# Performance work log

Hardware: AMD Instinct MI355X
Metric: run time of the kernel (lower is better)

Reference implementation:

```python
import jax, jax.numpy as jnp
import numpy as np

KEY_CHANNELS = 256


def conv1x1_relu(x, w, b):
    # x: [B, Cin, H, W], w: [Cout, Cin], b: [Cout] -> [B, Cout, H, W]
    y = jnp.einsum('oc,bchw->bohw', w, x) + b[None, :, None, None]
    return jax.nn.relu(y)


def setup_inputs() -> dict:
    key = jax.random.key(0)
    ks = jax.random.split(key, 16)
    B, C, H, W = 8, 512, 128, 128
    Kc, Kp = KEY_CHANNELS, 150
    sc = lambda cin: 1.0 / np.sqrt(cin)
    return {
        'x': jax.random.normal(ks[0], (B, C, H, W), jnp.float32),
        'proxy': jax.random.normal(ks[1], (B, C, Kp, 1), jnp.float32),
        'w_fp1': jax.random.normal(ks[2], (Kc, C), jnp.float32) * sc(C),
        'b_fp1': jax.random.normal(ks[3], (Kc,), jnp.float32) * 0.1,
        'w_fp2': jax.random.normal(ks[4], (Kc, Kc), jnp.float32) * sc(Kc),
        'b_fp2': jax.random.normal(ks[5], (Kc,), jnp.float32) * 0.1,
        'w_fo1': jax.random.normal(ks[6], (Kc, C), jnp.float32) * sc(C),
        'b_fo1': jax.random.normal(ks[7], (Kc,), jnp.float32) * 0.1,
        'w_fo2': jax.random.normal(ks[8], (Kc, Kc), jnp.float32) * sc(Kc),
        'b_fo2': jax.random.normal(ks[9], (Kc,), jnp.float32) * 0.1,
        'w_fd': jax.random.normal(ks[10], (Kc, C), jnp.float32) * sc(C),
        'b_fd': jax.random.normal(ks[11], (Kc,), jnp.float32) * 0.1,
        'w_fu': jax.random.normal(ks[12], (C, Kc), jnp.float32) * sc(Kc),
        'b_fu': jax.random.normal(ks[13], (C,), jnp.float32) * 0.1,
    }


def reference(x, proxy, w_fp1, b_fp1, w_fp2, b_fp2, w_fo1, b_fo1,
              w_fo2, b_fo2, w_fd, b_fd, w_fu, b_fu):
    B, C, H, W = x.shape
    Kc = w_fp1.shape[0]
    # f_pixel: two 1x1 conv(+folded BN)+ReLU blocks -> query [B, HW, Kc]
    q = conv1x1_relu(conv1x1_relu(x, w_fp1, b_fp1), w_fp2, b_fp2)
    query = q.reshape(B, Kc, H * W).transpose(0, 2, 1)
    # f_object -> key [B, Kc, Kp]
    k = conv1x1_relu(conv1x1_relu(proxy, w_fo1, b_fo1), w_fo2, b_fo2)
    key = k.reshape(B, Kc, -1)
    # f_down -> value [B, Kp, Kc]
    v = conv1x1_relu(proxy, w_fd, b_fd)
    value = v.reshape(B, Kc, -1).transpose(0, 2, 1)
    # cross-attention: softmax(Q K^T / sqrt(Kc)) V
    sim = jnp.einsum('bnc,bck->bnk', query, key) * (Kc ** -0.5)
    sim = jax.nn.softmax(sim, axis=-1)
    context = jnp.einsum('bnk,bkc->bnc', sim, value)  # [B, HW, Kc]
    context = context.transpose(0, 2, 1).reshape(B, Kc, H, W)
    # f_up: 1x1 conv(+folded BN)+ReLU back to in_channels
    return conv1x1_relu(context, w_fu, b_fu)
```

## Files before the change

### kernel.cpp

```cpp
#include <hip/hip_runtime.h>
#include <hip/hip_bf16.h>


typedef __bf16 bf16x8 __attribute__((ext_vector_type(8)));
typedef float f32x4 __attribute__((ext_vector_type(4)));
typedef unsigned short u16x8 __attribute__((ext_vector_type(8)));

#define MFMA_16x16x32(a, b, c) __builtin_amdgcn_mfma_f32_16x16x32_bf16((a), (b), (c), 0, 0, 0)

__device__ __forceinline__ unsigned short f2bf(float f) {
  union { float f; unsigned u; } x; x.f = f;
  unsigned r = (x.u + 0x7FFFu + ((x.u >> 16) & 1u)) >> 16;
  return (unsigned short)r;
}

__global__ __launch_bounds__(256) void cast_f32_bf16(const float* __restrict__ s,
                                                     unsigned short* __restrict__ d, int n) {
  int i = blockIdx.x * 256 + threadIdx.x;
  if (i < n) d[i] = f2bf(s[i]);
}

__global__ __launch_bounds__(256) void transpose_cast_x(const float* __restrict__ x,
                                                        unsigned short* __restrict__ xT) {
  const int HW = 16384, C = 512;
  __shared__ float tile[64][65];
  const int b = blockIdx.z;
  const int p0 = blockIdx.x * 64, c0 = blockIdx.y * 64;
  const int t = threadIdx.x;
#pragma unroll
  for (int i = 0; i < 4; i++) {
    int chunk = t + i * 256;
    int cl = chunk >> 4, q = chunk & 15;
    float4 v = *(const float4*)(x + ((size_t)b * C + c0 + cl) * HW + p0 + q * 4);
    tile[cl][q * 4 + 0] = v.x; tile[cl][q * 4 + 1] = v.y;
    tile[cl][q * 4 + 2] = v.z; tile[cl][q * 4 + 3] = v.w;
  }
  __syncthreads();
  {
    int pl = t >> 2, g = t & 3;
    u16x8 o0, o1;
#pragma unroll
    for (int j = 0; j < 8; j++) {
      o0[j] = f2bf(tile[g * 16 + j][pl]);
      o1[j] = f2bf(tile[g * 16 + 8 + j][pl]);
    }
    unsigned short* dst = xT + ((size_t)b * HW + p0 + pl) * C + c0 + g * 16;
    *(u16x8*)dst = o0;
    *(u16x8*)(dst + 8) = o1;
  }
}

__global__ __launch_bounds__(256) void kv_kernel(
    const float* __restrict__ proxy,
    const float* __restrict__ w_fo1, const float* __restrict__ b_fo1,
    const float* __restrict__ w_fo2, const float* __restrict__ b_fo2,
    const float* __restrict__ w_fd, const float* __restrict__ b_fd,
    unsigned short* __restrict__ keyT, unsigned short* __restrict__ Vv) {
  __shared__ float cols[512][8];
  __shared__ float k1s[256][8];
  const int b = blockIdx.y;
  const int p0 = blockIdx.x * 8;
  const int t = threadIdx.x;
#pragma unroll
  for (int i = 0; i < 8; i++) {
    int idx = t + i * 256;
    int c = idx >> 2, q = idx & 3;
    int p = p0 + q * 2;
    float2 v = make_float2(0.f, 0.f);
    if (p < 150) v = *(const float2*)(proxy + ((size_t)b * 512 + c) * 150 + p);
    cols[c][q * 2 + 0] = v.x;
    cols[c][q * 2 + 1] = v.y;
  }
  __syncthreads();
  float accV[8], accK[8];
  {
    float bv = b_fd[t], bk = b_fo1[t];
#pragma unroll
    for (int px = 0; px < 8; px++) { accV[px] = bv; accK[px] = bk; }
  }
#define KV_FMA(j, wv_, wk_)                                      \
  { float4 ca = *(const float4*)&cols[c + j][0];                 \
    float4 cb = *(const float4*)&cols[c + j][4];                 \
    accV[0] += wv_ * ca.x; accV[1] += wv_ * ca.y;                \
    accV[2] += wv_ * ca.z; accV[3] += wv_ * ca.w;                \
    accV[4] += wv_ * cb.x; accV[5] += wv_ * cb.y;                \
    accV[6] += wv_ * cb.z; accV[7] += wv_ * cb.w;                \
    accK[0] += wk_ * ca.x; accK[1] += wk_ * ca.y;                \
    accK[2] += wk_ * ca.z; accK[3] += wk_ * ca.w;                \
    accK[4] += wk_ * cb.x; accK[5] += wk_ * cb.y;                \
    accK[6] += wk_ * cb.z; accK[7] += wk_ * cb.w; }
  for (int c = 0; c < 512; c += 4) {
    float4 wv4 = *(const float4*)(w_fd + (size_t)t * 512 + c);
    float4 wk4 = *(const float4*)(w_fo1 + (size_t)t * 512 + c);
    KV_FMA(0, wv4.x, wk4.x)
    KV_FMA(1, wv4.y, wk4.y)
    KV_FMA(2, wv4.z, wk4.z)
    KV_FMA(3, wv4.w, wk4.w)
  }
#pragma unroll
  for (int px = 0; px < 8; px++) {
    Vv[((size_t)b * 256 + t) * 160 + p0 + px] = f2bf(fmaxf(accV[px], 0.f));
    k1s[t][px] = fmaxf(accK[px], 0.f);
  }
  __syncthreads();
  float accY[8];
  {
    float by = b_fo2[t];
#pragma unroll
    for (int px = 0; px < 8; px++) accY[px] = by;
  }
#define KV_FMA2(j, wy_)                                          \
  { float4 ca = *(const float4*)&k1s[c + j][0];                  \
    float4 cb = *(const float4*)&k1s[c + j][4];                  \
    accY[0] += wy_ * ca.x; accY[1] += wy_ * ca.y;                \
    accY[2] += wy_ * ca.z; accY[3] += wy_ * ca.w;                \
    accY[4] += wy_ * cb.x; accY[5] += wy_ * cb.y;                \
    accY[6] += wy_ * cb.z; accY[7] += wy_ * cb.w; }
  for (int c = 0; c < 256; c += 4) {
    float4 wy4 = *(const float4*)(w_fo2 + (size_t)t * 256 + c);
    KV_FMA2(0, wy4.x)
    KV_FMA2(1, wy4.y)
    KV_FMA2(2, wy4.z)
    KV_FMA2(3, wy4.w)
  }
#pragma unroll
  for (int px = 0; px < 8; px++)
    keyT[((size_t)b * 160 + p0 + px) * 256 + t] = f2bf(fmaxf(accY[px], 0.f));
}

template <int BIAS_ROW, int OUTF32>
__global__ __launch_bounds__(256, 4) void gemm_bt_relu(
    const unsigned short* __restrict__ A, const unsigned short* __restrict__ Bt,
    const float* __restrict__ bias, void* __restrict__ Cout,
    int M, int N, int K, long long sA, long long sB, long long sC) {
  __shared__ unsigned short As[128 * 64];
  __shared__ unsigned short Bs[128 * 64];
  const int b = blockIdx.z;
  const int m0 = blockIdx.x * 128, n0 = blockIdx.y * 128;
  const int tid = threadIdx.x;
  const int w = tid >> 6, l = tid & 63;
  const int lr = l & 15, lg = l >> 4;
  const int wm = (w >> 1) * 64, wn = (w & 1) * 64;
  const unsigned short* Ab = A + (size_t)b * sA + (size_t)m0 * K;
  const unsigned short* Btb = Bt + (size_t)b * sB + (size_t)n0 * K;
  const f32x4 zero = {0.f, 0.f, 0.f, 0.f};
  f32x4 acc[4][4];
#pragma unroll
  for (int m = 0; m < 4; m++)
#pragma unroll
    for (int n = 0; n < 4; n++) acc[m][n] = zero;

  const int srow = w * 32 + (l >> 3);
  const int scol = (l & 7) * 8;
  for (int kt = 0; kt < K; kt += 64) {
    __syncthreads();
#pragma unroll
    for (int i = 0; i < 4; i++) {
      __builtin_amdgcn_global_load_lds(
          (__attribute__((address_space(1))) void*)(Ab + (size_t)(srow + i * 8) * K + kt + scol),
          (__attribute__((address_space(3))) void*)(As + (w * 32 + i * 8) * 64), 16, 0, 0);
      __builtin_amdgcn_global_load_lds(
          (__attribute__((address_space(1))) void*)(Btb + (size_t)(srow + i * 8) * K + kt + scol),
          (__attribute__((address_space(3))) void*)(Bs + (w * 32 + i * 8) * 64), 16, 0, 0);
    }
    __syncthreads();
#pragma unroll
    for (int ks = 0; ks < 2; ks++) {
      bf16x8 aF[4], bF[4];
#pragma unroll
      for (int m = 0; m < 4; m++)
        aF[m] = *(const bf16x8*)(As + (wm + m * 16 + lr) * 64 + ks * 32 + lg * 8);
#pragma unroll
      for (int n = 0; n < 4; n++)
        bF[n] = *(const bf16x8*)(Bs + (wn + n * 16 + lr) * 64 + ks * 32 + lg * 8);
#pragma unroll
      for (int m = 0; m < 4; m++)
#pragma unroll
        for (int n = 0; n < 4; n++) acc[m][n] = MFMA_16x16x32(aF[m], bF[n], acc[m][n]);
    }
  }
#pragma unroll
  for (int m = 0; m < 4; m++) {
#pragma unroll
    for (int n = 0; n < 4; n++) {
      const int col = n0 + wn + n * 16 + lr;
      const float bc = BIAS_ROW ? 0.f : bias[col];
#pragma unroll
      for (int r = 0; r < 4; r++) {
        const int row = m0 + wm + m * 16 + lg * 4 + r;
        float v = acc[m][n][r] + (BIAS_ROW ? bias[row] : bc);
        v = fmaxf(v, 0.f);
        if (OUTF32)
          ((float*)Cout)[(size_t)b * sC + (size_t)row * N + col] = v;
        else
          ((unsigned short*)Cout)[(size_t)b * sC + (size_t)row * N + col] = f2bf(v);
      }
    }
  }
}

__global__ __launch_bounds__(256, 4) void attn_kernel(
    const unsigned short* __restrict__ Q, const unsigned short* __restrict__ Kt,
    const unsigned short* __restrict__ Vv, unsigned short* __restrict__ ctxT) {
  const int HW = 16384;
  __shared__ unsigned short Pls[128 * 160];
  const int b = blockIdx.y;
  const int pix0 = blockIdx.x * 128;
  const int tid = threadIdx.x;
  const int w = tid >> 6, l = tid & 63;
  const int lr = l & 15, lg = l >> 4;
  const unsigned short* Qb = Q + ((size_t)b * HW + pix0 + w * 32) * 256;
  const unsigned short* Kb = Kt + (size_t)b * 160 * 256;
  const unsigned short* Vb = Vv + (size_t)b * 256 * 160;
  const f32x4 zero = {0.f, 0.f, 0.f, 0.f};

  f32x4 acc[2][10];
#pragma unroll
  for (int m = 0; m < 2; m++)
#pragma unroll
    for (int n = 0; n < 10; n++) acc[m][n] = zero;
#pragma unroll 2
  for (int ks = 0; ks < 8; ks++) {
    bf16x8 aF[2];
#pragma unroll
    for (int m = 0; m < 2; m++)
      aF[m] = *(const bf16x8*)(Qb + (size_t)(m * 16 + lr) * 256 + ks * 32 + lg * 8);
#pragma unroll
    for (int n = 0; n < 10; n++) {
      bf16x8 bF = *(const bf16x8*)(Kb + (size_t)(n * 16 + lr) * 256 + ks * 32 + lg * 8);
      acc[0][n] = MFMA_16x16x32(aF[0], bF, acc[0][n]);
      acc[1][n] = MFMA_16x16x32(aF[1], bF, acc[1][n]);
    }
  }
  const float scale = 0.0625f;
#pragma unroll
  for (int m = 0; m < 2; m++) {
#pragma unroll
    for (int r = 0; r < 4; r++) {
      float lm = -1e30f;
#pragma unroll
      for (int n = 0; n < 10; n++) {
        float v = acc[m][n][r] * scale;
        acc[m][n][r] = v;
        if (n * 16 + lr < 150) lm = fmaxf(lm, v);
      }
#pragma unroll
      for (int msk = 1; msk <= 8; msk <<= 1) lm = fmaxf(lm, __shfl_xor(lm, msk, 64));
      float s = 0.f;
#pragma unroll
      for (int n = 0; n < 10; n++) {
        float p = (n * 16 + lr < 150) ? __expf(acc[m][n][r] - lm) : 0.f;
        acc[m][n][r] = p;
        s += p;
      }
#pragma unroll
      for (int msk = 1; msk <= 8; msk <<= 1) s += __shfl_xor(s, msk, 64);
      float inv = 1.f / s;
      const int row = w * 32 + m * 16 + lg * 4 + r;
      const unsigned sw = (unsigned)(row & 7) << 4;
#pragma unroll
      for (int n = 0; n < 10; n++) {
        unsigned boff = (unsigned)row * 320 + (unsigned)(n * 16 + lr) * 2;
        *(unsigned short*)((char*)Pls + (boff ^ sw)) = f2bf(acc[m][n][r] * inv);
      }
    }
  }
  __syncthreads();
  unsigned short* Cb = ctxT + ((size_t)b * HW + pix0 + w * 32) * 256;
#pragma unroll
  for (int half = 0; half < 2; half++) {
    f32x4 acc2[2][8];
#pragma unroll
    for (int m = 0; m < 2; m++)
#pragma unroll
      for (int n = 0; n < 8; n++) acc2[m][n] = zero;
    for (int ks = 0; ks < 5; ks++) {
      bf16x8 aP[2];
#pragma unroll
      for (int m = 0; m < 2; m++) {
        const int row = w * 32 + m * 16 + lr;
        unsigned boff = (unsigned)row * 320 + (unsigned)(ks * 64 + lg * 16);
        aP[m] = *(const bf16x8*)((const char*)Pls + (boff ^ ((unsigned)(row & 7) << 4)));
      }
#pragma unroll
      for (int n = 0; n < 8; n++) {
        const int ch = half * 128 + n * 16 + lr;
        bf16x8 bV = *(const bf16x8*)(Vb + (size_t)ch * 160 + ks * 32 + lg * 8);
        acc2[0][n] = MFMA_16x16x32(aP[0], bV, acc2[0][n]);
        acc2[1][n] = MFMA_16x16x32(aP[1], bV, acc2[1][n]);
      }
    }
#pragma unroll
    for (int m = 0; m < 2; m++)
#pragma unroll
      for (int n = 0; n < 8; n++)
#pragma unroll
        for (int r = 0; r < 4; r++)
          Cb[(size_t)(m * 16 + lg * 4 + r) * 256 + half * 128 + n * 16 + lr] =
              f2bf(acc2[m][n][r]);
  }
}

extern "C" void kernel_launch(void* const* d_in, const int* in_sizes, int n_in,
                              void* d_out, int out_size, void* d_ws, size_t ws_size,
                              hipStream_t stream) {
  (void)in_sizes; (void)n_in; (void)out_size;
  const float* x     = (const float*)d_in[0];
  const float* proxy = (const float*)d_in[1];
  const float* w_fp1 = (const float*)d_in[2];
  const float* b_fp1 = (const float*)d_in[3];
  const float* w_fp2 = (const float*)d_in[4];
  const float* b_fp2 = (const float*)d_in[5];
  const float* w_fo1 = (const float*)d_in[6];
  const float* b_fo1 = (const float*)d_in[7];
  const float* w_fo2 = (const float*)d_in[8];
  const float* b_fo2 = (const float*)d_in[9];
  const float* w_fd  = (const float*)d_in[10];
  const float* b_fd  = (const float*)d_in[11];
  const float* w_fu  = (const float*)d_in[12];
  const float* b_fu  = (const float*)d_in[13];

  char* ws = (char*)d_ws;
  unsigned short* W1b  = (unsigned short*)(ws + 0);
  unsigned short* W2b  = (unsigned short*)(ws + 262144);
  unsigned short* Wub  = (unsigned short*)(ws + 393216);
  unsigned short* keyT = (unsigned short*)(ws + 655360);
  unsigned short* Vv   = (unsigned short*)(ws + 1310720);
  unsigned short* bufA = (unsigned short*)(ws + 2097152);
  unsigned short* bufB = (unsigned short*)(ws + 2097152 + 134217728);
  if (ws_size < 203423744) return;

  dim3 blk(256);
  cast_f32_bf16<<<512, blk, 0, stream>>>(w_fp1, W1b, 131072);
  cast_f32_bf16<<<256, blk, 0, stream>>>(w_fp2, W2b, 65536);
  cast_f32_bf16<<<512, blk, 0, stream>>>(w_fu, Wub, 131072);
  transpose_cast_x<<<dim3(256, 8, 8), blk, 0, stream>>>(x, bufA);
  kv_kernel<<<dim3(20, 8), blk, 0, stream>>>(proxy, w_fo1, b_fo1, w_fo2, b_fo2,
                                             w_fd, b_fd, keyT, Vv);
  gemm_bt_relu<0, 0><<<dim3(128, 2, 8), blk, 0, stream>>>(
      bufA, W1b, b_fp1, bufB, 16384, 256, 512,
      (long long)16384 * 512, 0, (long long)16384 * 256);
  gemm_bt_relu<0, 0><<<dim3(128, 2, 8), blk, 0, stream>>>(
      bufB, W2b, b_fp2, bufA, 16384, 256, 256,
      (long long)16384 * 256, 0, (long long)16384 * 256);
  attn_kernel<<<dim3(128, 8), blk, 0, stream>>>(bufA, keyT, Vv, bufB);
  gemm_bt_relu<1, 1><<<dim3(4, 128, 8), blk, 0, stream>>>(
      Wub, bufB, b_fu, d_out, 512, 16384, 256,
      0, (long long)16384 * 256, (long long)512 * 16384);
}
```

Measured before the change: 428.7 us.

## Fuse x transpose-cast into first GEMM reading fp32 directly; merge weight casts

Removes the separate transpose_cast_x pass and has the first projection GEMM load fp32 x tiles straight from the channel-major layout into LDS. It uses a swizzled layout, then converts to bf16 while building MFMA fragments. The goal is to skip the extra write and read of a 128MB bf16 copy of x. The three weight cast launches are also merged into one kernel. The cost is scalar LDS reads with per-element conversion in the inner loop, twice the LDS footprint, and a block remap for L2 locality.

```diff
diff --git a/kernel.cpp b/kernel.cpp
--- a/kernel.cpp
+++ b/kernel.cpp
@@ -6,6 +6,8 @@
 typedef float f32x4 __attribute__((ext_vector_type(4)));
 typedef unsigned short u16x8 __attribute__((ext_vector_type(8)));
 
+#define AS1 __attribute__((address_space(1)))
+#define AS3 __attribute__((address_space(3)))
 #define MFMA_16x16x32(a, b, c) __builtin_amdgcn_mfma_f32_16x16x32_bf16((a), (b), (c), 0, 0, 0)
 
 __device__ __forceinline__ unsigned short f2bf(float f) {
@@ -14,40 +16,14 @@
   return (unsigned short)r;
 }
 
-__global__ __launch_bounds__(256) void cast_f32_bf16(const float* __restrict__ s,
-                                                     unsigned short* __restrict__ d, int n) {
+__global__ __launch_bounds__(256) void cast_weights(
+    const float* __restrict__ w1, const float* __restrict__ w2,
+    const float* __restrict__ wu, unsigned short* __restrict__ W1b,
+    unsigned short* __restrict__ W2b, unsigned short* __restrict__ Wub) {
   int i = blockIdx.x * 256 + threadIdx.x;
-  if (i < n) d[i] = f2bf(s[i]);
-}
-
-__global__ __launch_bounds__(256) void transpose_cast_x(const float* __restrict__ x,
-                                                        unsigned short* __restrict__ xT) {
-  const int HW = 16384, C = 512;
-  __shared__ float tile[64][65];
-  const int b = blockIdx.z;
-  const int p0 = blockIdx.x * 64, c0 = blockIdx.y * 64;
-  const int t = threadIdx.x;
-#pragma unroll
-  for (int i = 0; i < 4; i++) {
-    int chunk = t + i * 256;
-    int cl = chunk >> 4, q = chunk & 15;
-    float4 v = *(const float4*)(x + ((size_t)b * C + c0 + cl) * HW + p0 + q * 4);
-    tile[cl][q * 4 + 0] = v.x; tile[cl][q * 4 + 1] = v.y;
-    tile[cl][q * 4 + 2] = v.z; tile[cl][q * 4 + 3] = v.w;
-  }
-  __syncthreads();
-  {
-    int pl = t >> 2, g = t & 3;
-    u16x8 o0, o1;
-#pragma unroll
-    for (int j = 0; j < 8; j++) {
-      o0[j] = f2bf(tile[g * 16 + j][pl]);
-      o1[j] = f2bf(tile[g * 16 + 8 + j][pl]);
-    }
-    unsigned short* dst = xT + ((size_t)b * HW + p0 + pl) * C + c0 + g * 16;
-    *(u16x8*)dst = o0;
-    *(u16x8*)(dst + 8) = o1;
-  }
+  if (i < 131072) W1b[i] = f2bf(w1[i]);
+  else if (i < 196608) W2b[i - 131072] = f2bf(w2[i - 131072]);
+  else if (i < 327680) Wub[i - 196608] = f2bf(wu[i - 196608]);
 }
 
 __global__ __launch_bounds__(256) void kv_kernel(
@@ -128,6 +104,90 @@
     keyT[((size_t)b * 160 + p0 + px) * 256 + t] = f2bf(fmaxf(accY[px], 0.f));
 }
 
+__global__ __launch_bounds__(256, 3) void gemm1_fused(
+    const float* __restrict__ X, const unsigned short* __restrict__ Bt,
+    const float* __restrict__ bias, unsigned short* __restrict__ Cq) {
+  const int HW = 16384, K = 512, N = 256;
+  __shared__ float Af[64 * 128];
+  __shared__ unsigned short Bs[128 * 64];
+  const int r = blockIdx.x;
+  const int b = blockIdx.y;
+  const int my = ((r >> 4) << 3) | (r & 7);
+  const int nx = (r >> 3) & 1;
+  const int m0 = my * 128, n0 = nx * 128;
+  const int tid = threadIdx.x;
+  const int w = tid >> 6, l = tid & 63;
+  const int lr = l & 15, lg = l >> 4;
+  const int wm = (w >> 1) * 64, wn = (w & 1) * 64;
+  const float* Xb = X + (size_t)b * K * HW;
+  const unsigned short* Btb = Bt + (size_t)n0 * K;
+  const f32x4 zero = {0.f, 0.f, 0.f, 0.f};
+  f32x4 acc[4][4];
+#pragma unroll
+  for (int m = 0; m < 4; m++)
+#pragma unroll
+    for (int n = 0; n < 4; n++) acc[m][n] = zero;
+
+  const int arow = l >> 5;
+  const int acol = l & 31;
+  const int bsub = l >> 3;
+  const int bcol = (l & 7) * 8;
+  for (int kt = 0; kt < K; kt += 64) {
+    __syncthreads();
+#pragma unroll
+    for (int i = 0; i < 8; i++) {
+      const int rk = w * 16 + i * 2 + arow;
+      const int s = (rk >> 3) & 7;
+      __builtin_amdgcn_global_load_lds(
+          (AS1 void*)(Xb + (size_t)(kt + rk) * HW + m0 + ((acol ^ s) << 2)),
+          (AS3 void*)(Af + (w * 16 + i * 2) * 128), 16, 0, 0);
+    }
+#pragma unroll
+    for (int i = 0; i < 4; i++) {
+      __builtin_amdgcn_global_load_lds(
+          (AS1 void*)(Btb + (size_t)(w * 32 + i * 8 + bsub) * K + kt + bcol),
+          (AS3 void*)(Bs + (w * 32 + i * 8) * 64), 16, 0, 0);
+    }
+    __syncthreads();
+#pragma unroll
+    for (int ks = 0; ks < 2; ks++) {
+      bf16x8 aF[4], bF[4];
+      const int s = ks * 4 + lg;
+#pragma unroll
+      for (int m = 0; m < 4; m++) {
+        const int p = wm + m * 16 + lr;
+        const int cb = ((((p >> 2) ^ s) << 2) | (p & 3));
+        bf16x8 a;
+#pragma unroll
+        for (int j = 0; j < 8; j++)
+          a[j] = (__bf16)Af[(ks * 32 + lg * 8 + j) * 128 + cb];
+        aF[m] = a;
+      }
+#pragma unroll
+      for (int n = 0; n < 4; n++)
+        bF[n] = *(const bf16x8*)(Bs + (wn + n * 16 + lr) * 64 + ks * 32 + lg * 8);
+#pragma unroll
+      for (int m = 0; m < 4; m++)
+#pragma unroll
+        for (int n = 0; n < 4; n++) acc[m][n] = MFMA_16x16x32(aF[m], bF[n], acc[m][n]);
+    }
+  }
+  unsigned short* Cb = Cq + (size_t)b * HW * N;
+#pragma unroll
+  for (int m = 0; m < 4; m++) {
+#pragma unroll
+    for (int n = 0; n < 4; n++) {
+      const int col = n0 + wn + n * 16 + lr;
+      const float bc = bias[col];
+#pragma unroll
+      for (int r2 = 0; r2 < 4; r2++) {
+        const int row = m0 + wm + m * 16 + lg * 4 + r2;
+        Cb[(size_t)row * N + col] = f2bf(fmaxf(acc[m][n][r2] + bc, 0.f));
+      }
+    }
+  }
+}
+
 template <int BIAS_ROW, int OUTF32>
 __global__ __launch_bounds__(256, 4) void gemm_bt_relu(
     const unsigned short* __restrict__ A, const unsigned short* __restrict__ Bt,
@@ -157,11 +217,11 @@
 #pragma unroll
     for (int i = 0; i < 4; i++) {
       __builtin_amdgcn_global_load_lds(
-          (__attribute__((address_space(1))) void*)(Ab + (size_t)(srow + i * 8) * K + kt + scol),
-          (__attribute__((address_space(3))) void*)(As + (w * 32 + i * 8) * 64), 16, 0, 0);
+          (AS1 void*)(Ab + (size_t)(srow + i * 8) * K + kt + scol),
+          (AS3 void*)(As + (w * 32 + i * 8) * 64), 16, 0, 0);
       __builtin_amdgcn_global_load_lds(
-          (__attribute__((address_space(1))) void*)(Btb + (size_t)(srow + i * 8) * K + kt + scol),
-          (__attribute__((address_space(3))) void*)(Bs + (w * 32 + i * 8) * 64), 16, 0, 0);
+          (AS1 void*)(Btb + (size_t)(srow + i * 8) * K + kt + scol),
+          (AS3 void*)(Bs + (w * 32 + i * 8) * 64), 16, 0, 0);
     }
     __syncthreads();
 #pragma unroll
@@ -331,15 +391,10 @@
   if (ws_size < 203423744) return;
 
   dim3 blk(256);
-  cast_f32_bf16<<<512, blk, 0, stream>>>(w_fp1, W1b, 131072);
-  cast_f32_bf16<<<256, blk, 0, stream>>>(w_fp2, W2b, 65536);
-  cast_f32_bf16<<<512, blk, 0, stream>>>(w_fu, Wub, 131072);
-  transpose_cast_x<<<dim3(256, 8, 8), blk, 0, stream>>>(x, bufA);
+  cast_weights<<<1280, blk, 0, stream>>>(w_fp1, w_fp2, w_fu, W1b, W2b, Wub);
   kv_kernel<<<dim3(20, 8), blk, 0, stream>>>(proxy, w_fo1, b_fo1, w_fo2, b_fo2,
                                              w_fd, b_fd, keyT, Vv);
-  gemm_bt_relu<0, 0><<<dim3(128, 2, 8), blk, 0, stream>>>(
-      bufA, W1b, b_fp1, bufB, 16384, 256, 512,
-      (long long)16384 * 512, 0, (long long)16384 * 256);
+  gemm1_fused<<<dim3(256, 8), blk, 0, stream>>>(x, W1b, b_fp1, bufB);
   gemm_bt_relu<0, 0><<<dim3(128, 2, 8), blk, 0, stream>>>(
       bufB, W2b, b_fp2, bufA, 16384, 256, 256,
       (long long)16384 * 256, 0, (long long)16384 * 256);
```

Result: faster. 377.2 us (-12.0%).
